# Kernel tuning notes

Hardware: AMD Instinct MI355X
Metric: run time of the kernel (lower is better)

Reference implementation:

```python
import jax, jax.numpy as jnp
import numpy as np

ALPHA = 0.25
GAMMA = 2.0
EDGE_W = 1.0
NODE_W = 1.0

N = 200_000
E = 12_800_000
N_GRAPHS = 16
N_INST = 1000


def setup_inputs() -> dict:
    key = jax.random.key(0)
    k1, k2, k3, k4, k5 = jax.random.split(key, 5)
    edge_logits = jax.random.normal(k1, (E,), dtype=jnp.float32)
    node_logits = jax.random.normal(k2, (N,), dtype=jnp.float32)
    batch = jnp.sort(jax.random.randint(k3, (N,), 0, N_GRAPHS, dtype=jnp.int64) if jax.config.read('jax_enable_x64') else jax.random.randint(k3, (N,), 0, N_GRAPHS, dtype=jnp.int32))
    point_instances = jax.random.randint(k4, (N,), 0, N_INST, dtype=jnp.int32)
    edge_index = jax.random.randint(k5, (2, E), 0, N, dtype=jnp.int32)
    return {"edge_logits": edge_logits, "node_logits": node_logits,
            "batch": batch, "point_instances": point_instances,
            "edge_index": edge_index}


def _bce_with_logits(x, t):
    # numerically stable elementwise BCE-with-logits (reduction='none')
    return jnp.maximum(x, 0.0) - x * t + jnp.log1p(jnp.exp(-jnp.abs(x)))


def _sigmoid_focal_loss(x, t, alpha, gamma):
    # torchvision.ops.sigmoid_focal_loss, reduction='mean'
    p = jax.nn.sigmoid(x)
    ce = _bce_with_logits(x, t)
    p_t = p * t + (1.0 - p) * (1.0 - t)
    loss = ce * (1.0 - p_t) ** gamma
    alpha_t = alpha * t + (1.0 - alpha) * (1.0 - t)
    return jnp.mean(alpha_t * loss)


def _accuracy(x, t):
    # sigmoid > 0.5 -> 1 else 0 (note: == 0.5 maps to 0, as in the original)
    pred = (jax.nn.sigmoid(x) > 0.5).astype(x.dtype)
    return jnp.mean((pred == t).astype(jnp.float32))


def reference(edge_logits, node_logits, batch, point_instances, edge_index):
    src, dst = edge_index[0], edge_index[1]
    pi_s = point_instances[src]
    pi_d = point_instances[dst]
    # edge-wise equivalent of the original N x N mask gathered at edge_index:
    # same instance AND same graph AND both instances nonzero
    same = (pi_s == pi_d) & (batch[src] == batch[dst]) & (pi_s != 0) & (pi_d != 0)
    edge_targets = same.astype(jnp.float32)  # [E]

    edge_loss = _sigmoid_focal_loss(edge_logits, edge_targets, ALPHA, GAMMA)
    edge_acc = _accuracy(edge_logits, edge_targets)

    node_targets = (point_instances != 0).astype(jnp.float32)  # [N]
    node_loss = _sigmoid_focal_loss(node_logits, node_targets, ALPHA, GAMMA)
    node_acc = _accuracy(node_logits, node_targets)

    loss = EDGE_W * edge_loss + NODE_W * node_loss
    return loss, edge_loss, node_loss, edge_acc, node_acc
```

## Files before the change

### kernel.cpp

```cpp
#include <hip/hip_runtime.h>
#include <limits.h>


typedef int   iv4 __attribute__((ext_vector_type(4)));
typedef float fv4 __attribute__((ext_vector_type(4)));

#define MAX_PART 4096

__device__ __forceinline__ float focal_term(float x, int t) {
    float y = t ? -x : x;
    float e = __expf(-fabsf(y));
    float ce = fmaxf(y, 0.f) + __logf(1.f + e);
    float inv = __builtin_amdgcn_rcpf(1.f + e);
    float sg = (y >= 0.f) ? inv : e * inv;
    float w = t ? 0.25f : 0.75f;
    return w * ce * sg * sg;
}

__device__ __forceinline__ float acc_term(float x, int t) {
    return ((x > 0.f) == (t != 0)) ? 1.f : 0.f;
}

__device__ __forceinline__ void block_reduce_out(float v0, float v1,
                                                 float* a0, float* a1,
                                                 float2* part) {
#pragma unroll
    for (int off = 32; off > 0; off >>= 1) {
        v0 += __shfl_down(v0, off, 64);
        v1 += __shfl_down(v1, off, 64);
    }
    __shared__ float s0[8], s1[8];
    int wave = threadIdx.x >> 6;
    int lane = threadIdx.x & 63;
    if (lane == 0) { s0[wave] = v0; s1[wave] = v1; }
    __syncthreads();
    if (threadIdx.x == 0) {
        int nw = blockDim.x >> 6;
        float t0 = 0.f, t1 = 0.f;
        for (int w = 0; w < nw; ++w) { t0 += s0[w]; t1 += s1[w]; }
        if (part) {
            part[blockIdx.x] = make_float2(t0, t1);
        } else {
            atomicAdd(a0, t0);
            atomicAdd(a1, t1);
        }
    }
}

__global__ void node_key_kernel(const float* __restrict__ nl,
                                const int* __restrict__ batch,
                                const int* __restrict__ pi,
                                int N, unsigned short* __restrict__ key,
                                int* __restrict__ bnd,
                                float* __restrict__ acc,
                                float2* __restrict__ part) {
    int tid = blockIdx.x * blockDim.x + threadIdx.x;
    int nthreads = gridDim.x * blockDim.x;
    int C = N >> 3;
    float ls = 0.f, ac = 0.f;
    const iv4* pi4 = reinterpret_cast<const iv4*>(pi);
    const iv4* b4  = reinterpret_cast<const iv4*>(batch);
    const fv4* nl4 = reinterpret_cast<const fv4*>(nl);

    for (int c = tid; c < C; c += nthreads) {
        int base = c << 3;
        iv4 p0 = pi4[(c << 1) + 0], p1 = pi4[(c << 1) + 1];
        iv4 b0 = b4[(c << 1) + 0],  b1 = b4[(c << 1) + 1];
        fv4 x0 = nl4[(c << 1) + 0], x1 = nl4[(c << 1) + 1];
        int pv[8] = {p0.x, p0.y, p0.z, p0.w, p1.x, p1.y, p1.z, p1.w};
        int bv[8] = {b0.x, b0.y, b0.z, b0.w, b1.x, b1.y, b1.z, b1.w};
        float xv[8] = {x0.x, x0.y, x0.z, x0.w, x1.x, x1.y, x1.z, x1.w};
        int bp = (base > 0) ? batch[base - 1] : -1;
        unsigned int kv[8];
#pragma unroll
        for (int j = 0; j < 8; ++j) {
            int p = pv[j];
            int t = (p != 0) ? 1 : 0;
            int b = bv[j];
            kv[j] = t ? (unsigned int)((b << 10) | p) : 0u;
            if (bp != b) {
                for (int k = bp + 1; k <= b; ++k) bnd[k] = base + j;
            }
            bp = b;
            ls += focal_term(xv[j], t);
            ac += acc_term(xv[j], t);
        }
        if (base + 8 == N) {
            for (int k = bv[7] + 1; k <= 16; ++k) bnd[k] = N;
        }
        iv4 kp;
        kp.x = (int)(kv[0] | (kv[1] << 16));
        kp.y = (int)(kv[2] | (kv[3] << 16));
        kp.z = (int)(kv[4] | (kv[5] << 16));
        kp.w = (int)(kv[6] | (kv[7] << 16));
        reinterpret_cast<iv4*>(key)[c] = kp;
    }
    if (tid == 0) {
        for (int i = C << 3; i < N; ++i) {
            int p = pi[i];
            int t = (p != 0) ? 1 : 0;
            int b = batch[i];
            key[i] = t ? (unsigned short)((b << 10) | p) : (unsigned short)0;
            if (i == 0) {
                for (int k = 0; k <= b; ++k) bnd[k] = 0;
            } else {
                int bp = batch[i - 1];
                for (int k = bp + 1; k <= b; ++k) bnd[k] = i;
            }
            if (i == N - 1) {
                for (int k = b + 1; k <= 16; ++k) bnd[k] = N;
            }
            float x = nl[i];
            ls += focal_term(x, t);
            ac += acc_term(x, t);
        }
    }
    block_reduce_out(ls, ac, acc + 2, acc + 3, part);
}

__global__ void __launch_bounds__(256, 4)
edge_kernel_key(const float* __restrict__ el,
                const int* __restrict__ src,
                const int* __restrict__ dst,
                const unsigned short* __restrict__ key,
                const int* __restrict__ bnd_g,
                int E, float gscale, float* __restrict__ acc,
                float2* __restrict__ part) {
    __shared__ int bnd[17];
    if (threadIdx.x < 17) bnd[threadIdx.x] = bnd_g[threadIdx.x];
    __syncthreads();

    const int G16 = E >> 4;
    int tid = blockIdx.x * blockDim.x + threadIdx.x;
    int stride = gridDim.x * blockDim.x;
    float ls = 0.f, ac = 0.f;
    const iv4* src4 = reinterpret_cast<const iv4*>(src);
    const iv4* dst4 = reinterpret_cast<const iv4*>(dst);
    const fv4* el4  = reinterpret_cast<const fv4*>(el);

    for (int g = tid; g < G16; g += stride) {
        int base = g << 2;
        int si[16], di[16];
#pragma unroll
        for (int j = 0; j < 4; ++j) {
            iv4 s = __builtin_nontemporal_load(src4 + base + j);
            iv4 d = __builtin_nontemporal_load(dst4 + base + j);
            si[j * 4 + 0] = s.x; si[j * 4 + 1] = s.y;
            si[j * 4 + 2] = s.z; si[j * 4 + 3] = s.w;
            di[j * 4 + 0] = d.x; di[j * 4 + 1] = d.y;
            di[j * 4 + 2] = d.z; di[j * 4 + 3] = d.w;
        }
        unsigned int sameMask = 0;
#pragma unroll
        for (int i = 0; i < 16; ++i) {
            int s = si[i], d = di[i];
            int gg = (int)((float)s * gscale);
            gg = gg < 0 ? 0 : (gg > 15 ? 15 : gg);
            int lo = bnd[gg], hi = bnd[gg + 1];
            while (s < lo) { --gg; hi = lo; lo = bnd[gg]; }
            while (s >= hi) { ++gg; lo = hi; hi = bnd[gg + 1]; }
            int same = (d >= lo) & (d < hi);
            sameMask |= (unsigned int)same << i;
            si[i] = same ? s : 0;
            di[i] = same ? d : 0;
        }
        unsigned short ks[16], kd[16];
#pragma unroll
        for (int i = 0; i < 16; ++i) ks[i] = key[si[i]];
#pragma unroll
        for (int i = 0; i < 16; ++i) kd[i] = key[di[i]];
        float xv[16];
#pragma unroll
        for (int j = 0; j < 4; ++j) {
            fv4 x = __builtin_nontemporal_load(el4 + base + j);
            xv[j * 4 + 0] = x.x; xv[j * 4 + 1] = x.y;
            xv[j * 4 + 2] = x.z; xv[j * 4 + 3] = x.w;
        }
#pragma unroll
        for (int i = 0; i < 16; ++i) {
            int t = (int)((sameMask >> i) & 1u) & (ks[i] == kd[i]) & (ks[i] != 0);
            ls += focal_term(xv[i], t);
            ac += acc_term(xv[i], t);
        }
    }
    if (tid == 0) {
        for (int i = (G16 << 4); i < E; ++i) {
            int s = src[i], d = dst[i];
            int gg = (int)((float)s * gscale);
            gg = gg < 0 ? 0 : (gg > 15 ? 15 : gg);
            int lo = bnd[gg], hi = bnd[gg + 1];
            while (s < lo) { --gg; hi = lo; lo = bnd[gg]; }
            while (s >= hi) { ++gg; lo = hi; hi = bnd[gg + 1]; }
            int same = (d >= lo) & (d < hi);
            unsigned short ks = key[same ? s : 0], kd = key[same ? d : 0];
            int t = same & (ks == kd) & (ks != 0);
            float x = el[i];
            ls += focal_term(x, t);
            ac += acc_term(x, t);
        }
    }
    block_reduce_out(ls, ac, acc + 0, acc + 1, part);
}

__global__ void edge_kernel_direct(const float* __restrict__ el,
                                   const int* __restrict__ src,
                                   const int* __restrict__ dst,
                                   const int* __restrict__ batch,
                                   const int* __restrict__ pi,
                                   int E, float* __restrict__ acc) {
    int G = E >> 2;
    int stride = gridDim.x * blockDim.x;
    int tid = blockIdx.x * blockDim.x + threadIdx.x;
    float ls = 0.f, ac = 0.f;
    for (int g = tid; g < G; g += stride) {
        float4 x = reinterpret_cast<const float4*>(el)[g];
        int4 s = reinterpret_cast<const int4*>(src)[g];
        int4 d = reinterpret_cast<const int4*>(dst)[g];
        int is[4] = {s.x, s.y, s.z, s.w};
        int id[4] = {d.x, d.y, d.z, d.w};
        float xs[4] = {x.x, x.y, x.z, x.w};
#pragma unroll
        for (int j = 0; j < 4; ++j) {
            int ps = pi[is[j]], pd = pi[id[j]];
            int t = (ps == pd) & (batch[is[j]] == batch[id[j]]) & (ps != 0);
            ls += focal_term(xs[j], t);
            ac += acc_term(xs[j], t);
        }
    }
    if (tid == 0) {
        for (int i = (G << 2); i < E; ++i) {
            int ps = pi[src[i]], pd = pi[dst[i]];
            int t = (ps == pd) & (batch[src[i]] == batch[dst[i]]) & (ps != 0);
            float x = el[i];
            ls += focal_term(x, t);
            ac += acc_term(x, t);
        }
    }
    block_reduce_out(ls, ac, acc + 0, acc + 1, nullptr);
}

__global__ void finalize_kernel(const float* __restrict__ acc,
                                const float2* __restrict__ epart, int ne,
                                const float2* __restrict__ npart, int nn,
                                int use_part,
                                float* __restrict__ out, int E, int N) {
    float el = 0.f, ea = 0.f, nl = 0.f, na = 0.f;
    if (use_part) {
        for (int i = threadIdx.x; i < ne; i += 256) {
            float2 p = epart[i];
            el += p.x; ea += p.y;
        }
        for (int i = threadIdx.x; i < nn; i += 256) {
            float2 p = npart[i];
            nl += p.x; na += p.y;
        }
#pragma unroll
        for (int off = 32; off > 0; off >>= 1) {
            el += __shfl_down(el, off, 64);
            ea += __shfl_down(ea, off, 64);
            nl += __shfl_down(nl, off, 64);
            na += __shfl_down(na, off, 64);
        }
        __shared__ float s[4][4];
        int wave = threadIdx.x >> 6;
        int lane = threadIdx.x & 63;
        if (lane == 0) {
            s[wave][0] = el; s[wave][1] = ea;
            s[wave][2] = nl; s[wave][3] = na;
        }
        __syncthreads();
        if (threadIdx.x == 0) {
            el = 0.f; ea = 0.f; nl = 0.f; na = 0.f;
            for (int w = 0; w < 4; ++w) {
                el += s[w][0]; ea += s[w][1];
                nl += s[w][2]; na += s[w][3];
            }
            float invE = 1.f / (float)E;
            float invN = 1.f / (float)N;
            float elm = el * invE, eam = ea * invE;
            float nlm = nl * invN, nam = na * invN;
            out[0] = elm + nlm;
            out[1] = elm;
            out[2] = nlm;
            out[3] = eam;
            out[4] = nam;
        }
    } else if (threadIdx.x == 0) {
        float invE = 1.f / (float)E;
        float invN = 1.f / (float)N;
        float elm = acc[0] * invE;
        float eam = acc[1] * invE;
        float nlm = acc[2] * invN;
        float nam = acc[3] * invN;
        out[0] = elm + nlm;
        out[1] = elm;
        out[2] = nlm;
        out[3] = eam;
        out[4] = nam;
    }
}

extern "C" void kernel_launch(void* const* d_in, const int* in_sizes, int n_in,
                              void* d_out, int out_size, void* d_ws, size_t ws_size,
                              hipStream_t stream) {
    const float* edge_logits = (const float*)d_in[0];
    const float* node_logits = (const float*)d_in[1];
    const int*   batch       = (const int*)d_in[2];
    const int*   pinst       = (const int*)d_in[3];
    const int*   eidx        = (const int*)d_in[4];
    const int E = in_sizes[0];
    const int N = in_sizes[1];
    const int* src = eidx;
    const int* dst = eidx + E;
    float* out = (float*)d_out;

    float* acc = (float*)d_ws;
    int*   bnd = (int*)((char*)d_ws + 64);
    unsigned short* key = (unsigned short*)((char*)d_ws + 256);
    size_t key_end = 256 + (size_t)N * sizeof(unsigned short);
    size_t part_off = (key_end + 255) & ~(size_t)255;
    float2* epart = (float2*)((char*)d_ws + part_off);
    float2* npart = epart + MAX_PART;
    size_t need_full = part_off + 2 * MAX_PART * sizeof(float2);

    const bool use_key  = (ws_size >= key_end);
    const bool use_part = (ws_size >= need_full);

    const int block = 256;
    int C = N >> 3;
    int node_grid = (C + block - 1) / block;
    if (node_grid < 1) node_grid = 1;
    if (node_grid > MAX_PART) node_grid = MAX_PART;

    if (!use_part) {
        (void)hipMemsetAsync(d_ws, 0, 16, stream);
    }

    node_key_kernel<<<node_grid, block, 0, stream>>>(
        node_logits, batch, pinst, N, key, bnd, acc,
        use_part ? npart : nullptr);

    int G16 = E >> 4;
    int edge_grid = (G16 + block - 1) / block;
    if (edge_grid < 1) edge_grid = 1;
    if (edge_grid > MAX_PART) edge_grid = MAX_PART;

    if (use_key) {
        float gscale = 16.0f / (float)N;
        edge_kernel_key<<<edge_grid, block, 0, stream>>>(
            edge_logits, src, dst, key, bnd, E, gscale, acc,
            use_part ? epart : nullptr);
    } else {
        int G = E >> 2;
        int eg = (G + block - 1) / block;
        if (eg > 65535 * 4) eg = 65535 * 4;
        if (eg < 1) eg = 1;
        edge_kernel_direct<<<eg, block, 0, stream>>>(edge_logits, src, dst,
                                                     batch, pinst, E, acc);
    }

    finalize_kernel<<<1, 256, 0, stream>>>(acc, epart, edge_grid,
                                           npart, node_grid,
                                           (use_key && use_part) ? 1 : 0,
                                           out, E, N);
}
```

Baseline: 218.0 us.

## Split edge loss into dense negative pass plus sparse positive correction

Computes every edge's focal and accuracy term as if its target were zero, fused into the node kernel that also builds keys. The keyed edge kernel then only gathers logits for edges whose target is one and adds the difference. This removes the logit stream and most transcendental work from the gather-bound edge kernel, and moves that streaming into the first kernel. The fallback path is also simplified to per-element kernels with wave-level atomics.

```diff
diff --git a/kernel.cpp b/kernel.cpp
--- a/kernel.cpp
+++ b/kernel.cpp
@@ -21,9 +21,7 @@
     return ((x > 0.f) == (t != 0)) ? 1.f : 0.f;
 }
 
-__device__ __forceinline__ void block_reduce_out(float v0, float v1,
-                                                 float* a0, float* a1,
-                                                 float2* part) {
+__device__ __forceinline__ void block_store2(float v0, float v1, float2* part) {
 #pragma unroll
     for (int off = 32; off > 0; off >>= 1) {
         v0 += __shfl_down(v0, off, 64);
@@ -38,31 +36,53 @@
         int nw = blockDim.x >> 6;
         float t0 = 0.f, t1 = 0.f;
         for (int w = 0; w < nw; ++w) { t0 += s0[w]; t1 += s1[w]; }
-        if (part) {
-            part[blockIdx.x] = make_float2(t0, t1);
-        } else {
-            atomicAdd(a0, t0);
-            atomicAdd(a1, t1);
-        }
-    }
-}
-
-__global__ void node_key_kernel(const float* __restrict__ nl,
-                                const int* __restrict__ batch,
-                                const int* __restrict__ pi,
-                                int N, unsigned short* __restrict__ key,
-                                int* __restrict__ bnd,
-                                float* __restrict__ acc,
-                                float2* __restrict__ part) {
+        part[blockIdx.x] = make_float2(t0, t1);
+    }
+}
+
+__device__ __forceinline__ void block_store4(float v0, float v1, float v2,
+                                             float v3, float4* part) {
+#pragma unroll
+    for (int off = 32; off > 0; off >>= 1) {
+        v0 += __shfl_down(v0, off, 64);
+        v1 += __shfl_down(v1, off, 64);
+        v2 += __shfl_down(v2, off, 64);
+        v3 += __shfl_down(v3, off, 64);
+    }
+    __shared__ float s[4][8];
+    int wave = threadIdx.x >> 6;
+    int lane = threadIdx.x & 63;
+    if (lane == 0) { s[0][wave] = v0; s[1][wave] = v1;
+                     s[2][wave] = v2; s[3][wave] = v3; }
+    __syncthreads();
+    if (threadIdx.x == 0) {
+        int nw = blockDim.x >> 6;
+        float t0 = 0.f, t1 = 0.f, t2 = 0.f, t3 = 0.f;
+        for (int w = 0; w < nw; ++w) {
+            t0 += s[0][w]; t1 += s[1][w]; t2 += s[2][w]; t3 += s[3][w];
+        }
+        part[blockIdx.x] = make_float4(t0, t1, t2, t3);
+    }
+}
+
+__global__ void __launch_bounds__(256, 4)
+node_e1_kernel(const float* __restrict__ nl,
+               const int* __restrict__ batch,
+               const int* __restrict__ pi,
+               int N,
+               const float* __restrict__ el, int E,
+               unsigned short* __restrict__ key,
+               int* __restrict__ bnd,
+               float4* __restrict__ part) {
     int tid = blockIdx.x * blockDim.x + threadIdx.x;
-    int nthreads = gridDim.x * blockDim.x;
+    int nth = gridDim.x * blockDim.x;
+    float nls = 0.f, nac = 0.f, els = 0.f, eac = 0.f;
+
     int C = N >> 3;
-    float ls = 0.f, ac = 0.f;
     const iv4* pi4 = reinterpret_cast<const iv4*>(pi);
     const iv4* b4  = reinterpret_cast<const iv4*>(batch);
     const fv4* nl4 = reinterpret_cast<const fv4*>(nl);
-
-    for (int c = tid; c < C; c += nthreads) {
+    for (int c = tid; c < C; c += nth) {
         int base = c << 3;
         iv4 p0 = pi4[(c << 1) + 0], p1 = pi4[(c << 1) + 1];
         iv4 b0 = b4[(c << 1) + 0],  b1 = b4[(c << 1) + 1];
@@ -82,8 +102,8 @@
                 for (int k = bp + 1; k <= b; ++k) bnd[k] = base + j;
             }
             bp = b;
-            ls += focal_term(xv[j], t);
-            ac += acc_term(xv[j], t);
+            nls += focal_term(xv[j], t);
+            nac += acc_term(xv[j], t);
         }
         if (base + 8 == N) {
             for (int k = bv[7] + 1; k <= 16; ++k) bnd[k] = N;
@@ -111,34 +131,57 @@
                 for (int k = b + 1; k <= 16; ++k) bnd[k] = N;
             }
             float x = nl[i];
-            ls += focal_term(x, t);
-            ac += acc_term(x, t);
-        }
-    }
-    block_reduce_out(ls, ac, acc + 2, acc + 3, part);
+            nls += focal_term(x, t);
+            nac += acc_term(x, t);
+        }
+    }
+
+    int G16 = E >> 4;
+    const fv4* el4 = reinterpret_cast<const fv4*>(el);
+    for (int g = tid; g < G16; g += nth) {
+        int base = g << 2;
+        fv4 y0 = __builtin_nontemporal_load(el4 + base + 0);
+        fv4 y1 = __builtin_nontemporal_load(el4 + base + 1);
+        fv4 y2 = __builtin_nontemporal_load(el4 + base + 2);
+        fv4 y3 = __builtin_nontemporal_load(el4 + base + 3);
+        float xv[16] = {y0.x, y0.y, y0.z, y0.w, y1.x, y1.y, y1.z, y1.w,
+                        y2.x, y2.y, y2.z, y2.w, y3.x, y3.y, y3.z, y3.w};
+#pragma unroll
+        for (int i = 0; i < 16; ++i) {
+            els += focal_term(xv[i], 0);
+            eac += acc_term(xv[i], 0);
+        }
+    }
+    if (tid == 0) {
+        for (int i = G16 << 4; i < E; ++i) {
+            float x = el[i];
+            els += focal_term(x, 0);
+            eac += acc_term(x, 0);
+        }
+    }
+    block_store4(nls, nac, els, eac, part);
 }
 
 __global__ void __launch_bounds__(256, 4)
-edge_kernel_key(const float* __restrict__ el,
-                const int* __restrict__ src,
-                const int* __restrict__ dst,
-                const unsigned short* __restrict__ key,
-                const int* __restrict__ bnd_g,
-                int E, float gscale, float* __restrict__ acc,
-                float2* __restrict__ part) {
+edge_corr_kernel(const int* __restrict__ src,
+                 const int* __restrict__ dst,
+                 const float* __restrict__ el,
+                 const unsigned short* __restrict__ key,
+                 const int* __restrict__ bnd_g,
+                 int E, float gscale,
+                 float2* __restrict__ part) {
     __shared__ int bnd[17];
     if (threadIdx.x < 17) bnd[threadIdx.x] = bnd_g[threadIdx.x];
     __syncthreads();
 
     const int G16 = E >> 4;
     int tid = blockIdx.x * blockDim.x + threadIdx.x;
-    int stride = gridDim.x * blockDim.x;
+    int nth = gridDim.x * blockDim.x;
     float ls = 0.f, ac = 0.f;
     const iv4* src4 = reinterpret_cast<const iv4*>(src);
     const iv4* dst4 = reinterpret_cast<const iv4*>(dst);
-    const fv4* el4  = reinterpret_cast<const fv4*>(el);
-
-    for (int g = tid; g < G16; g += stride) {
+
+    for (int g = tid; g < G16; g += nth) {
         int base = g << 2;
         int si[16], di[16];
 #pragma unroll
@@ -169,18 +212,22 @@
         for (int i = 0; i < 16; ++i) ks[i] = key[si[i]];
 #pragma unroll
         for (int i = 0; i < 16; ++i) kd[i] = key[di[i]];
-        float xv[16];
-#pragma unroll
-        for (int j = 0; j < 4; ++j) {
-            fv4 x = __builtin_nontemporal_load(el4 + base + j);
-            xv[j * 4 + 0] = x.x; xv[j * 4 + 1] = x.y;
-            xv[j * 4 + 2] = x.z; xv[j * 4 + 3] = x.w;
-        }
+        unsigned int tmask = 0;
 #pragma unroll
         for (int i = 0; i < 16; ++i) {
             int t = (int)((sameMask >> i) & 1u) & (ks[i] == kd[i]) & (ks[i] != 0);
-            ls += focal_term(xv[i], t);
-            ac += acc_term(xv[i], t);
+            tmask |= (unsigned int)t << i;
+        }
+        if (tmask) {
+            int ebase = g << 4;
+            unsigned int tm = tmask;
+            do {
+                int i = (int)__builtin_ctz(tm);
+                tm &= tm - 1;
+                float x = el[ebase + i];
+                ls += focal_term(x, 1) - focal_term(x, 0);
+                ac += (x > 0.f) ? 1.f : -1.f;
+            } while (tm);
         }
     }
     if (tid == 0) {
@@ -194,12 +241,36 @@
             int same = (d >= lo) & (d < hi);
             unsigned short ks = key[same ? s : 0], kd = key[same ? d : 0];
             int t = same & (ks == kd) & (ks != 0);
-            float x = el[i];
-            ls += focal_term(x, t);
-            ac += acc_term(x, t);
-        }
-    }
-    block_reduce_out(ls, ac, acc + 0, acc + 1, part);
+            if (t) {
+                float x = el[i];
+                ls += focal_term(x, 1) - focal_term(x, 0);
+                ac += (x > 0.f) ? 1.f : -1.f;
+            }
+        }
+    }
+    block_store2(ls, ac, part);
+}
+
+__global__ void node_atomic_kernel(const float* __restrict__ nl,
+                                   const int* __restrict__ pi,
+                                   int N, float* __restrict__ acc) {
+    int stride = gridDim.x * blockDim.x;
+    float ls = 0.f, ac = 0.f;
+    for (int i = blockIdx.x * blockDim.x + threadIdx.x; i < N; i += stride) {
+        int t = (pi[i] != 0) ? 1 : 0;
+        float x = nl[i];
+        ls += focal_term(x, t);
+        ac += acc_term(x, t);
+    }
+#pragma unroll
+    for (int off = 32; off > 0; off >>= 1) {
+        ls += __shfl_down(ls, off, 64);
+        ac += __shfl_down(ac, off, 64);
+    }
+    if ((threadIdx.x & 63) == 0) {
+        atomicAdd(acc + 2, ls);
+        atomicAdd(acc + 3, ac);
+    }
 }
 
 __global__ void edge_kernel_direct(const float* __restrict__ el,
@@ -208,77 +279,64 @@
                                    const int* __restrict__ batch,
                                    const int* __restrict__ pi,
                                    int E, float* __restrict__ acc) {
-    int G = E >> 2;
     int stride = gridDim.x * blockDim.x;
-    int tid = blockIdx.x * blockDim.x + threadIdx.x;
     float ls = 0.f, ac = 0.f;
-    for (int g = tid; g < G; g += stride) {
-        float4 x = reinterpret_cast<const float4*>(el)[g];
-        int4 s = reinterpret_cast<const int4*>(src)[g];
-        int4 d = reinterpret_cast<const int4*>(dst)[g];
-        int is[4] = {s.x, s.y, s.z, s.w};
-        int id[4] = {d.x, d.y, d.z, d.w};
-        float xs[4] = {x.x, x.y, x.z, x.w};
-#pragma unroll
-        for (int j = 0; j < 4; ++j) {
-            int ps = pi[is[j]], pd = pi[id[j]];
-            int t = (ps == pd) & (batch[is[j]] == batch[id[j]]) & (ps != 0);
-            ls += focal_term(xs[j], t);
-            ac += acc_term(xs[j], t);
-        }
-    }
-    if (tid == 0) {
-        for (int i = (G << 2); i < E; ++i) {
-            int ps = pi[src[i]], pd = pi[dst[i]];
-            int t = (ps == pd) & (batch[src[i]] == batch[dst[i]]) & (ps != 0);
-            float x = el[i];
-            ls += focal_term(x, t);
-            ac += acc_term(x, t);
-        }
-    }
-    block_reduce_out(ls, ac, acc + 0, acc + 1, nullptr);
+    for (int i = blockIdx.x * blockDim.x + threadIdx.x; i < E; i += stride) {
+        int ps = pi[src[i]], pd = pi[dst[i]];
+        int t = (ps == pd) & (batch[src[i]] == batch[dst[i]]) & (ps != 0);
+        float x = el[i];
+        ls += focal_term(x, t);
+        ac += acc_term(x, t);
+    }
+#pragma unroll
+    for (int off = 32; off > 0; off >>= 1) {
+        ls += __shfl_down(ls, off, 64);
+        ac += __shfl_down(ac, off, 64);
+    }
+    if ((threadIdx.x & 63) == 0) {
+        atomicAdd(acc + 0, ls);
+        atomicAdd(acc + 1, ac);
+    }
 }
 
 __global__ void finalize_kernel(const float* __restrict__ acc,
-                                const float2* __restrict__ epart, int ne,
-                                const float2* __restrict__ npart, int nn,
+                                const float4* __restrict__ p1, int n1,
+                                const float2* __restrict__ p2, int n2,
                                 int use_part,
                                 float* __restrict__ out, int E, int N) {
-    float el = 0.f, ea = 0.f, nl = 0.f, na = 0.f;
     if (use_part) {
-        for (int i = threadIdx.x; i < ne; i += 256) {
-            float2 p = epart[i];
-            el += p.x; ea += p.y;
-        }
-        for (int i = threadIdx.x; i < nn; i += 256) {
-            float2 p = npart[i];
-            nl += p.x; na += p.y;
+        float nls = 0.f, nac = 0.f, els = 0.f, eac = 0.f;
+        for (int i = threadIdx.x; i < n1; i += 256) {
+            float4 p = p1[i];
+            nls += p.x; nac += p.y; els += p.z; eac += p.w;
+        }
+        for (int i = threadIdx.x; i < n2; i += 256) {
+            float2 p = p2[i];
+            els += p.x; eac += p.y;
         }
 #pragma unroll
         for (int off = 32; off > 0; off >>= 1) {
-            el += __shfl_down(el, off, 64);
-            ea += __shfl_down(ea, off, 64);
-            nl += __shfl_down(nl, off, 64);
-            na += __shfl_down(na, off, 64);
+            nls += __shfl_down(nls, off, 64);
+            nac += __shfl_down(nac, off, 64);
+            els += __shfl_down(els, off, 64);
+            eac += __shfl_down(eac, off, 64);
         }
         __shared__ float s[4][4];
         int wave = threadIdx.x >> 6;
         int lane = threadIdx.x & 63;
-        if (lane == 0) {
-            s[wave][0] = el; s[wave][1] = ea;
-            s[wave][2] = nl; s[wave][3] = na;
-        }
+        if (lane == 0) { s[0][wave] = nls; s[1][wave] = nac;
+                         s[2][wave] = els; s[3][wave] = eac; }
         __syncthreads();
         if (threadIdx.x == 0) {
-            el = 0.f; ea = 0.f; nl = 0.f; na = 0.f;
+            nls = 0.f; nac = 0.f; els = 0.f; eac = 0.f;
             for (int w = 0; w < 4; ++w) {
-                el += s[w][0]; ea += s[w][1];
-                nl += s[w][2]; na += s[w][3];
+                nls += s[0][w]; nac += s[1][w];
+                els += s[2][w]; eac += s[3][w];
             }
             float invE = 1.f / (float)E;
             float invN = 1.f / (float)N;
-            float elm = el * invE, eam = ea * invE;
-            float nlm = nl * invN, nam = na * invN;
+            float elm = els * invE, eam = eac * invE;
+            float nlm = nls * invN, nam = nac * invN;
             out[0] = elm + nlm;
             out[1] = elm;
             out[2] = nlm;
@@ -319,48 +377,42 @@
     unsigned short* key = (unsigned short*)((char*)d_ws + 256);
     size_t key_end = 256 + (size_t)N * sizeof(unsigned short);
     size_t part_off = (key_end + 255) & ~(size_t)255;
-    float2* epart = (float2*)((char*)d_ws + part_off);
-    float2* npart = epart + MAX_PART;
-    size_t need_full = part_off + 2 * MAX_PART * sizeof(float2);
-
-    const bool use_key  = (ws_size >= key_end);
-    const bool use_part = (ws_size >= need_full);
-
+    float4* part1 = (float4*)((char*)d_ws + part_off);
+    float2* part2 = (float2*)(part1 + MAX_PART);
+    size_t need_full = part_off + MAX_PART * (sizeof(float4) + sizeof(float2));
+
+    const bool full = (ws_size >= need_full);
     const int block = 256;
     int C = N >> 3;
-    int node_grid = (C + block - 1) / block;
-    if (node_grid < 1) node_grid = 1;
-    if (node_grid > MAX_PART) node_grid = MAX_PART;
-
-    if (!use_part) {
+    int G16 = E >> 4;
+
+    if (full) {
+        int g1 = (G16 + block - 1) / block;
+        int g1n = (C + block - 1) / block;
+        if (g1n > g1) g1 = g1n;
+        if (g1 < 1) g1 = 1;
+        if (g1 > MAX_PART) g1 = MAX_PART;
+        int g2 = (G16 + block - 1) / block;
+        if (g2 < 1) g2 = 1;
+        if (g2 > MAX_PART) g2 = MAX_PART;
+
+        node_e1_kernel<<<g1, block, 0, stream>>>(node_logits, batch, pinst, N,
+                                                 edge_logits, E, key, bnd, part1);
+        float gscale = 16.0f / (float)N;
+        edge_corr_kernel<<<g2, block, 0, stream>>>(src, dst, edge_logits, key,
+                                                   bnd, E, gscale, part2);
+        finalize_kernel<<<1, 256, 0, stream>>>(acc, part1, g1, part2, g2, 1,
+                                               out, E, N);
+    } else {
         (void)hipMemsetAsync(d_ws, 0, 16, stream);
-    }
-
-    node_key_kernel<<<node_grid, block, 0, stream>>>(
-        node_logits, batch, pinst, N, key, bnd, acc,
-        use_part ? npart : nullptr);
-
-    int G16 = E >> 4;
-    int edge_grid = (G16 + block - 1) / block;
-    if (edge_grid < 1) edge_grid = 1;
-    if (edge_grid > MAX_PART) edge_grid = MAX_PART;
-
-    if (use_key) {
-        float gscale = 16.0f / (float)N;
-        edge_kernel_key<<<edge_grid, block, 0, stream>>>(
-            edge_logits, src, dst, key, bnd, E, gscale, acc,
-            use_part ? epart : nullptr);
-    } else {
-        int G = E >> 2;
-        int eg = (G + block - 1) / block;
-        if (eg > 65535 * 4) eg = 65535 * 4;
-        if (eg < 1) eg = 1;
+        int ng = (N + block - 1) / block;
+        if (ng > 2048) ng = 2048;
+        node_atomic_kernel<<<ng, block, 0, stream>>>(node_logits, pinst, N, acc);
+        int eg = (E + block - 1) / block;
+        if (eg > 2048) eg = 2048;
         edge_kernel_direct<<<eg, block, 0, stream>>>(edge_logits, src, dst,
                                                      batch, pinst, E, acc);
-    }
-
-    finalize_kernel<<<1, 256, 0, stream>>>(acc, epart, edge_grid,
-                                           npart, node_grid,
-                                           (use_key && use_part) ? 1 : 0,
-                                           out, E, N);
-}
+        finalize_kernel<<<1, 256, 0, stream>>>(acc, part1, 0, part2, 0, 0,
+                                               out, E, N);
+    }
+}
```

After: 220.0 us. Within noise of the previous version (+0.9%).
